# Kernel optimization log

Hardware: AMD Instinct MI355X
Metric: run time of the kernel (lower is better)

The kernel has to match this reference:

```python
import jax, jax.numpy as jnp
import numpy as np

N_OBS = 2_097_152
N_BAND = 4
T_SPAN = 3650.0  # days


def setup_inputs() -> dict:
    key = jax.random.key(0)
    k0, k1, k2, k3, k4, k5 = jax.random.split(key, 6)
    t = jnp.sort(jax.random.uniform(k0, (N_OBS,), jnp.float32) * T_SPAN)
    band = jax.random.randint(k1, (N_OBS,), 0, N_BAND)
    y = jax.random.normal(k2, (N_OBS,), jnp.float32)
    yerr = 0.1 + 0.9 * jax.random.uniform(k3, (N_OBS,), jnp.float32)
    log_amp_delta = 0.1 * jax.random.normal(k4, (N_BAND - 1,), jnp.float32)
    # [log sigma, log ell] for the quasisep Exp kernel
    log_kernel_param = jnp.array([0.0, np.log(50.0)], dtype=jnp.float32) + \
        0.1 * jax.random.normal(k5, (2,), jnp.float32)
    return {"t": t, "band": band, "y": y, "yerr": yerr,
            "log_amp_delta": log_amp_delta, "log_kernel_param": log_kernel_param}


def _log_prob(t, band, y, yerr, log_amp_delta, log_kernel_param):
    # amp_transform: prepend 0 -> per-band amplitudes
    amps = jnp.exp(jnp.concatenate([jnp.zeros(1, log_amp_delta.dtype), log_amp_delta]))
    sigma2 = jnp.exp(2.0 * log_kernel_param[0])
    ell = jnp.exp(log_kernel_param[1])

    # lag_transform with zero lags: sort by time (assume_sorted path of tinygp)
    inds = jnp.argsort(t)
    ts, b = t[inds], band[inds]
    ys, dg = y[inds], (yerr ** 2)[inds]

    # multiband Exp kernel: K_ij = sigma2 * u_i * u_j * exp(-(t_i - t_j)/ell), i>=j
    u = amps[b]                       # per-point amplitude
    a = dg + sigma2 * u * u           # diagonal K_ii + noise
    U = sigma2 * u                    # semiseparable left factor
    V = u                             # semiseparable right factor
    dt = jnp.diff(ts)
    P = jnp.concatenate([jnp.zeros(1, ts.dtype), jnp.exp(-dt / ell)])  # decay factors

    # Celerite O(N) Cholesky (K = L D L^T) fused with the forward solve L z = y.
    def step(carry, x):
        cS, cg = carry                # cS = S_{n-1} + D_{n-1} W_{n-1}^2 ; cg = g_{n-1} + W_{n-1} z_{n-1}
        Pn, an, Un, Vn, yn = x
        Sn = Pn * Pn * cS
        gn = Pn * cg
        Dn = an - Un * Un * Sn
        Wn = (Vn - Sn * Un) / Dn
        zn = yn - Un * gn
        return (Sn + Dn * Wn * Wn, gn + Wn * zn), (jnp.log(Dn), zn * zn / Dn)

    zero = jnp.zeros((), ts.dtype)
    _, (logD, quad) = jax.lax.scan(step, (zero, zero), (P, a, U, V, ys))
    n = ts.shape[0]
    return -0.5 * (jnp.sum(quad) + jnp.sum(logD) + n * jnp.log(2.0 * jnp.pi))


def reference(t, band, y, yerr, log_amp_delta, log_kernel_param):
    return _log_prob(t, band, y, yerr, log_amp_delta, log_kernel_param)
```

## Files before the change

### kernel.cpp

```cpp
#include <hip/hip_runtime.h>
#include <math.h>

#define N_TOTAL 2097152
#define NT 256
#define NC 16
#define EPB (NT * NC)
#define NB (N_TOTAL / EPB)

struct DMat { double al, be, ga, de, c, e, f; };

__device__ __forceinline__ DMat dmat_identity() {
    DMat m; m.al = 1.0; m.be = 0.0; m.ga = 0.0; m.de = 1.0; m.c = 1.0; m.e = 0.0; m.f = 0.0;
    return m;
}

__device__ __forceinline__ DMat dmat_compose(const DMat& A, const DMat& B) {
    DMat r;
    r.al = A.al * B.al + A.be * B.ga;
    r.be = A.al * B.be + A.be * B.de;
    r.ga = A.ga * B.al + A.de * B.ga;
    r.de = A.ga * B.be + A.de * B.de;
    r.c  = A.c * B.c;
    r.e  = A.e * B.al + A.c * B.e + A.f * B.ga;
    r.f  = A.e * B.be + A.c * B.f + A.f * B.de;
    return r;
}

__device__ __forceinline__ void dmat_normalize(DMat& m) {
    double mx = fmax(fabs(m.al), fabs(m.be));
    mx = fmax(mx, fabs(m.ga));
    mx = fmax(mx, fabs(m.de));
    mx = fmax(mx, fabs(m.c));
    mx = fmax(mx, fabs(m.e));
    mx = fmax(mx, fabs(m.f));
    if (!(mx > 0.0) || isinf(mx)) return;
    double inv = 1.0 / mx;
    m.al *= inv; m.be *= inv; m.ga *= inv; m.de *= inv;
    m.c *= inv; m.e *= inv; m.f *= inv;
}

__device__ __forceinline__ void dmat_store(double* sm, int i, const DMat& m) {
    sm[0 * NT + i] = m.al; sm[1 * NT + i] = m.be; sm[2 * NT + i] = m.ga;
    sm[3 * NT + i] = m.de; sm[4 * NT + i] = m.c;  sm[5 * NT + i] = m.e;
    sm[6 * NT + i] = m.f;
}

__device__ __forceinline__ DMat dmat_load(const double* sm, int i) {
    DMat m;
    m.al = sm[0 * NT + i]; m.be = sm[1 * NT + i]; m.ga = sm[2 * NT + i];
    m.de = sm[3 * NT + i]; m.c  = sm[4 * NT + i]; m.e  = sm[5 * NT + i];
    m.f  = sm[6 * NT + i];
    return m;
}

__device__ __forceinline__ DMat dmat_scan_inclusive(double* sm, DMat mine, int tid) {
    dmat_store(sm, tid, mine);
    __syncthreads();
    for (int d = 1; d < NT; d <<= 1) {
        DMat o;
        bool has = (tid >= d);
        if (has) o = dmat_load(sm, tid - d);
        __syncthreads();
        if (has) {
            mine = dmat_compose(mine, o);
            dmat_normalize(mine);
            dmat_store(sm, tid, mine);
        }
        __syncthreads();
    }
    return mine;
}

__device__ __forceinline__ DMat elem_mat(double P, double a, double U, double V, double yy) {
    double p = P * P;
    DMat m;
    m.al = p * (a - 2.0 * U * V);
    m.be = V * V;
    m.ga = -(p * U * U);
    m.de = a;
    m.c  = P * (a - U * V);
    m.e  = -(yy * p * U);
    m.f  = yy * V;
    return m;
}

__global__ __launch_bounds__(NT) void k_upsweep(
    const float* __restrict__ t, const int* __restrict__ band,
    const float* __restrict__ y, const float* __restrict__ yerr,
    const float* __restrict__ lad, const float* __restrict__ lkp,
    double* __restrict__ block_comp)
{
    __shared__ double sm[7 * NT];
    const int tid = threadIdx.x;
    const double sigma2 = exp(2.0 * (double)lkp[0]);
    const double inv_ell = exp(-(double)lkp[1]);
    double amps[4];
    amps[0] = 1.0;
    amps[1] = exp((double)lad[0]);
    amps[2] = exp((double)lad[1]);
    amps[3] = exp((double)lad[2]);

    const int base = (blockIdx.x * NT + tid) * NC;
    double tprev = (base == 0) ? 0.0 : (double)t[base - 1];
    DMat acc = dmat_identity();
    #pragma unroll
    for (int k = 0; k < NC; k += 4) {
        float4 tv = *reinterpret_cast<const float4*>(t + base + k);
        float4 yv = *reinterpret_cast<const float4*>(y + base + k);
        float4 ev = *reinterpret_cast<const float4*>(yerr + base + k);
        int4   bv = *reinterpret_cast<const int4*>(band + base + k);
        float tc[4] = {tv.x, tv.y, tv.z, tv.w};
        float yc[4] = {yv.x, yv.y, yv.z, yv.w};
        float ec[4] = {ev.x, ev.y, ev.z, ev.w};
        int   bc[4] = {bv.x, bv.y, bv.z, bv.w};
        #pragma unroll
        for (int j = 0; j < 4; ++j) {
            double u = amps[bc[j] & 3];
            double a = (double)ec[j] * (double)ec[j] + sigma2 * u * u;
            double U = sigma2 * u;
            double P = ((base + k + j) == 0) ? 0.0
                     : exp(-((double)tc[j] - tprev) * inv_ell);
            acc = dmat_compose(elem_mat(P, a, U, u, (double)yc[j]), acc);
            tprev = (double)tc[j];
        }
    }
    dmat_normalize(acc);
    DMat incl = dmat_scan_inclusive(sm, acc, tid);
    if (tid == NT - 1) {
        double* o = block_comp + blockIdx.x * 7;
        o[0] = incl.al; o[1] = incl.be; o[2] = incl.ga; o[3] = incl.de;
        o[4] = incl.c;  o[5] = incl.e;  o[6] = incl.f;
    }
}

__global__ __launch_bounds__(NT) void k_spine(
    const double* __restrict__ block_comp, double* __restrict__ block_excl)
{
    __shared__ double sm[7 * NT];
    const int tid = threadIdx.x;
    const double* p0 = block_comp + (2 * tid) * 7;
    const double* p1 = block_comp + (2 * tid + 1) * 7;
    DMat m0 = {p0[0], p0[1], p0[2], p0[3], p0[4], p0[5], p0[6]};
    DMat m1 = {p1[0], p1[1], p1[2], p1[3], p1[4], p1[5], p1[6]};
    DMat mine = dmat_compose(m1, m0);
    dmat_normalize(mine);
    dmat_scan_inclusive(sm, mine, tid);
    DMat E = (tid == 0) ? dmat_identity() : dmat_load(sm, tid - 1);
    double* o0 = block_excl + (2 * tid) * 7;
    o0[0] = E.al; o0[1] = E.be; o0[2] = E.ga; o0[3] = E.de;
    o0[4] = E.c;  o0[5] = E.e;  o0[6] = E.f;
    DMat M = dmat_compose(m0, E);
    dmat_normalize(M);
    double* o1 = block_excl + (2 * tid + 1) * 7;
    o1[0] = M.al; o1[1] = M.be; o1[2] = M.ga; o1[3] = M.de;
    o1[4] = M.c;  o1[5] = M.e;  o1[6] = M.f;
}

__global__ __launch_bounds__(NT) void k_replay(
    const float* __restrict__ t, const int* __restrict__ band,
    const float* __restrict__ y, const float* __restrict__ yerr,
    const float* __restrict__ lad, const float* __restrict__ lkp,
    const double* __restrict__ block_excl, double* __restrict__ accum)
{
    __shared__ double sm[7 * NT];
    const int tid = threadIdx.x;
    const double sigma2 = exp(2.0 * (double)lkp[0]);
    const double inv_ell = exp(-(double)lkp[1]);
    double amps[4];
    amps[0] = 1.0;
    amps[1] = exp((double)lad[0]);
    amps[2] = exp((double)lad[1]);
    amps[3] = exp((double)lad[2]);

    const int base = (blockIdx.x * NT + tid) * NC;
    double tprev = (base == 0) ? 0.0 : (double)t[base - 1];

    double Pv[NC];
    float av[NC], Uv[NC], Vv[NC], yv_[NC];
    DMat acc = dmat_identity();
    #pragma unroll
    for (int k = 0; k < NC; k += 4) {
        float4 tv = *reinterpret_cast<const float4*>(t + base + k);
        float4 yv = *reinterpret_cast<const float4*>(y + base + k);
        float4 ev = *reinterpret_cast<const float4*>(yerr + base + k);
        int4   bv = *reinterpret_cast<const int4*>(band + base + k);
        float tc[4] = {tv.x, tv.y, tv.z, tv.w};
        float yc[4] = {yv.x, yv.y, yv.z, yv.w};
        float ec[4] = {ev.x, ev.y, ev.z, ev.w};
        int   bc[4] = {bv.x, bv.y, bv.z, bv.w};
        #pragma unroll
        for (int j = 0; j < 4; ++j) {
            double u = amps[bc[j] & 3];
            double a = (double)ec[j] * (double)ec[j] + sigma2 * u * u;
            double U = sigma2 * u;
            double P = ((base + k + j) == 0) ? 0.0
                     : exp(-((double)tc[j] - tprev) * inv_ell);
            Pv[k + j] = P;
            av[k + j] = (float)a; Uv[k + j] = (float)U;
            Vv[k + j] = (float)u; yv_[k + j] = yc[j];
            acc = dmat_compose(elem_mat(P, a, U, u, (double)yc[j]), acc);
            tprev = (double)tc[j];
        }
    }
    dmat_normalize(acc);
    dmat_scan_inclusive(sm, acc, tid);
    DMat E = (tid == 0) ? dmat_identity() : dmat_load(sm, tid - 1);

    const double* pb = block_excl + blockIdx.x * 7;
    DMat Eb = {pb[0], pb[1], pb[2], pb[3], pb[4], pb[5], pb[6]};
    DMat F = dmat_compose(E, Eb);
    dmat_normalize(F);
    double x = 0.0, g = 0.0;
    if (F.de != 0.0 && !isinf(F.de)) {
        double invde = 1.0 / F.de;
        x = F.be * invde;
        g = F.f  * invde;
    }
    if (!isfinite(x)) x = 0.0;
    if (!isfinite(g)) g = 0.0;

    double s_logD = 0.0, s_quad = 0.0;
    #pragma unroll
    for (int k = 0; k < NC; ++k) {
        double P = Pv[k], a = (double)av[k], U = (double)Uv[k];
        double V = (double)Vv[k], yy = (double)yv_[k];
        double p = P * P;
        double S = p * x;
        double D = a - U * U * S;
        if (!(D > 1e-300)) D = 1e-300;
        double W = (V - S * U) / D;
        double gn = P * g;
        double z = yy - U * gn;
        s_logD += log(D);
        s_quad += z * z / D;
        x = S + D * W * W;
        g = gn + W * z;
    }

    __syncthreads();
    sm[tid] = s_logD;
    sm[NT + tid] = s_quad;
    __syncthreads();
    for (int d = NT / 2; d > 0; d >>= 1) {
        if (tid < d) {
            sm[tid] += sm[tid + d];
            sm[NT + tid] += sm[NT + tid + d];
        }
        __syncthreads();
    }
    if (tid == 0) {
        atomicAdd(&accum[0], sm[0]);
        atomicAdd(&accum[1], sm[NT]);
    }
}

__global__ void k_zero(double* __restrict__ accum) {
    accum[0] = 0.0;
    accum[1] = 0.0;
}

__global__ void k_final(const double* __restrict__ accum, float* __restrict__ out) {
    double r = -0.5 * (accum[0] + accum[1]
                       + (double)N_TOTAL * 1.8378770664093454836);
    out[0] = (float)r;
}

extern "C" void kernel_launch(void* const* d_in, const int* in_sizes, int n_in,
                              void* d_out, int out_size, void* d_ws, size_t ws_size,
                              hipStream_t stream)
{
    const float* t    = (const float*)d_in[0];
    const int*   band = (const int*)d_in[1];
    const float* y    = (const float*)d_in[2];
    const float* yerr = (const float*)d_in[3];
    const float* lad  = (const float*)d_in[4];
    const float* lkp  = (const float*)d_in[5];

    double* dws        = (double*)d_ws;
    double* block_comp = dws;
    double* block_excl = dws + NB * 7;
    double* accum      = dws + 2 * NB * 7;

    k_zero<<<1, 1, 0, stream>>>(accum);
    k_upsweep<<<NB, NT, 0, stream>>>(t, band, y, yerr, lad, lkp, block_comp);
    k_spine<<<1, NT, 0, stream>>>(block_comp, block_excl);
    k_replay<<<NB, NT, 0, stream>>>(t, band, y, yerr, lad, lkp, block_excl, accum);
    k_final<<<1, 1, 0, stream>>>(accum, (float*)d_out);
}
```

Baseline: 123.9 us.

## Store per-thread prefixes to skip matrix rescan in replay, split upsweep chains

The upsweep now writes every thread's inclusive prefix matrix to global memory in SoA layout. The replay kernel reads its predecessor's prefix instead of recomputing the per-element matrix compose and block scan. The upsweep runs two independent half-chains per thread for more ILP, and exponentials drop to float expf with branchless band amplitudes. Replay batches logs via a product of D, uses wave shuffles for the reduction, and fuses zero/final kernels via a done-counter, trading extra global traffic and some precision for less FP64 compute and fewer launches.

```diff
diff --git a/kernel.cpp b/kernel.cpp
--- a/kernel.cpp
+++ b/kernel.cpp
@@ -6,6 +6,7 @@
 #define NC 16
 #define EPB (NT * NC)
 #define NB (N_TOTAL / EPB)
+#define NTH (NB * NT)
 
 struct DMat { double al, be, ga, de, c, e, f; };
 
@@ -84,25 +85,156 @@
     return m;
 }
 
+__device__ __forceinline__ double band_amp(int b, double a1, double a2, double a3) {
+    double lo = (b & 1) ? a1 : 1.0;
+    double hi = (b & 1) ? a3 : a2;
+    return (b & 2) ? hi : lo;
+}
+
 __global__ __launch_bounds__(NT) void k_upsweep(
     const float* __restrict__ t, const int* __restrict__ band,
     const float* __restrict__ y, const float* __restrict__ yerr,
     const float* __restrict__ lad, const float* __restrict__ lkp,
-    double* __restrict__ block_comp)
+    double* __restrict__ ptc)
 {
     __shared__ double sm[7 * NT];
     const int tid = threadIdx.x;
     const double sigma2 = exp(2.0 * (double)lkp[0]);
-    const double inv_ell = exp(-(double)lkp[1]);
-    double amps[4];
-    amps[0] = 1.0;
-    amps[1] = exp((double)lad[0]);
-    amps[2] = exp((double)lad[1]);
-    amps[3] = exp((double)lad[2]);
-
-    const int base = (blockIdx.x * NT + tid) * NC;
-    double tprev = (base == 0) ? 0.0 : (double)t[base - 1];
-    DMat acc = dmat_identity();
+    const float inv_ell_f = expf(-lkp[1]);
+    const double amp1 = exp((double)lad[0]);
+    const double amp2 = exp((double)lad[1]);
+    const double amp3 = exp((double)lad[2]);
+
+    const int gid = blockIdx.x * NT + tid;
+    const int base = gid * NC;
+    const bool first = (base == 0);
+
+    float tpA = first ? 0.0f : t[base - 1];
+    float tpB = t[base + NC / 2 - 1];
+
+    DMat accA = dmat_identity();
+    DMat accB = dmat_identity();
+
+    #pragma unroll
+    for (int kk = 0; kk < NC / 2; kk += 4) {
+        float4 tvA = *reinterpret_cast<const float4*>(t + base + kk);
+        float4 yvA = *reinterpret_cast<const float4*>(y + base + kk);
+        float4 evA = *reinterpret_cast<const float4*>(yerr + base + kk);
+        int4   bvA = *reinterpret_cast<const int4*>(band + base + kk);
+        float4 tvB = *reinterpret_cast<const float4*>(t + base + NC / 2 + kk);
+        float4 yvB = *reinterpret_cast<const float4*>(y + base + NC / 2 + kk);
+        float4 evB = *reinterpret_cast<const float4*>(yerr + base + NC / 2 + kk);
+        int4   bvB = *reinterpret_cast<const int4*>(band + base + NC / 2 + kk);
+        float tA[4] = {tvA.x, tvA.y, tvA.z, tvA.w};
+        float yA[4] = {yvA.x, yvA.y, yvA.z, yvA.w};
+        float eA[4] = {evA.x, evA.y, evA.z, evA.w};
+        int   bA[4] = {bvA.x, bvA.y, bvA.z, bvA.w};
+        float tB[4] = {tvB.x, tvB.y, tvB.z, tvB.w};
+        float yB[4] = {yvB.x, yvB.y, yvB.z, yvB.w};
+        float eB[4] = {evB.x, evB.y, evB.z, evB.w};
+        int   bB[4] = {bvB.x, bvB.y, bvB.z, bvB.w};
+        #pragma unroll
+        for (int j = 0; j < 4; ++j) {
+            {
+                double u = band_amp(bA[j], amp1, amp2, amp3);
+                double U = sigma2 * u;
+                double a = (double)eA[j] * (double)eA[j] + U * u;
+                float dt = tA[j] - tpA; tpA = tA[j];
+                double P = (first && kk == 0 && j == 0)
+                         ? 0.0 : (double)expf(-dt * inv_ell_f);
+                accA = dmat_compose(elem_mat(P, a, U, u, (double)yA[j]), accA);
+            }
+            {
+                double u = band_amp(bB[j], amp1, amp2, amp3);
+                double U = sigma2 * u;
+                double a = (double)eB[j] * (double)eB[j] + U * u;
+                float dt = tB[j] - tpB; tpB = tB[j];
+                double P = (double)expf(-dt * inv_ell_f);
+                accB = dmat_compose(elem_mat(P, a, U, u, (double)yB[j]), accB);
+            }
+        }
+    }
+    DMat acc = dmat_compose(accB, accA);
+    dmat_normalize(acc);
+    DMat incl = dmat_scan_inclusive(sm, acc, tid);
+    ptc[0 * NTH + gid] = incl.al; ptc[1 * NTH + gid] = incl.be;
+    ptc[2 * NTH + gid] = incl.ga; ptc[3 * NTH + gid] = incl.de;
+    ptc[4 * NTH + gid] = incl.c;  ptc[5 * NTH + gid] = incl.e;
+    ptc[6 * NTH + gid] = incl.f;
+}
+
+__global__ __launch_bounds__(NT) void k_spine(
+    const double* __restrict__ ptc, double* __restrict__ block_excl,
+    double* __restrict__ accum, unsigned int* __restrict__ done)
+{
+    __shared__ double sm[7 * NT];
+    const int tid = threadIdx.x;
+    if (tid == 0) { accum[0] = 0.0; accum[1] = 0.0; *done = 0u; }
+    const int g0 = (2 * tid) * NT + (NT - 1);
+    const int g1 = (2 * tid + 1) * NT + (NT - 1);
+    DMat m0 = {ptc[0 * NTH + g0], ptc[1 * NTH + g0], ptc[2 * NTH + g0],
+               ptc[3 * NTH + g0], ptc[4 * NTH + g0], ptc[5 * NTH + g0],
+               ptc[6 * NTH + g0]};
+    DMat m1 = {ptc[0 * NTH + g1], ptc[1 * NTH + g1], ptc[2 * NTH + g1],
+               ptc[3 * NTH + g1], ptc[4 * NTH + g1], ptc[5 * NTH + g1],
+               ptc[6 * NTH + g1]};
+    DMat mine = dmat_compose(m1, m0);
+    dmat_normalize(mine);
+    dmat_scan_inclusive(sm, mine, tid);
+    DMat E = (tid == 0) ? dmat_identity() : dmat_load(sm, tid - 1);
+    double* o0 = block_excl + (2 * tid) * 7;
+    o0[0] = E.al; o0[1] = E.be; o0[2] = E.ga; o0[3] = E.de;
+    o0[4] = E.c;  o0[5] = E.e;  o0[6] = E.f;
+    DMat M = dmat_compose(m0, E);
+    dmat_normalize(M);
+    double* o1 = block_excl + (2 * tid + 1) * 7;
+    o1[0] = M.al; o1[1] = M.be; o1[2] = M.ga; o1[3] = M.de;
+    o1[4] = M.c;  o1[5] = M.e;  o1[6] = M.f;
+}
+
+__global__ __launch_bounds__(NT) void k_replay(
+    const float* __restrict__ t, const int* __restrict__ band,
+    const float* __restrict__ y, const float* __restrict__ yerr,
+    const float* __restrict__ lad, const float* __restrict__ lkp,
+    const double* __restrict__ ptc, const double* __restrict__ block_excl,
+    double* __restrict__ accum, unsigned int* __restrict__ done,
+    float* __restrict__ out)
+{
+    const int tid = threadIdx.x;
+    const int gid = blockIdx.x * NT + tid;
+    const double sigma2 = exp(2.0 * (double)lkp[0]);
+    const float inv_ell_f = expf(-lkp[1]);
+    const double amp1 = exp((double)lad[0]);
+    const double amp2 = exp((double)lad[1]);
+    const double amp3 = exp((double)lad[2]);
+
+    const double* pb = block_excl + blockIdx.x * 7;
+    DMat Eb = {pb[0], pb[1], pb[2], pb[3], pb[4], pb[5], pb[6]};
+    DMat F;
+    if (tid == 0) {
+        F = Eb;
+    } else {
+        const int gm1 = gid - 1;
+        DMat E = {ptc[0 * NTH + gm1], ptc[1 * NTH + gm1], ptc[2 * NTH + gm1],
+                  ptc[3 * NTH + gm1], ptc[4 * NTH + gm1], ptc[5 * NTH + gm1],
+                  ptc[6 * NTH + gm1]};
+        F = dmat_compose(E, Eb);
+    }
+    dmat_normalize(F);
+    double x = 0.0, g = 0.0;
+    if (F.de != 0.0 && !isinf(F.de)) {
+        double invde = 1.0 / F.de;
+        x = F.be * invde;
+        g = F.f  * invde;
+    }
+    if (!isfinite(x)) x = 0.0;
+    if (!isfinite(g)) g = 0.0;
+
+    const int base = gid * NC;
+    const bool first = (base == 0);
+    float tp = first ? 0.0f : t[base - 1];
+
+    double s_logD = 0.0, s_quad = 0.0, pd = 1.0;
     #pragma unroll
     for (int k = 0; k < NC; k += 4) {
         float4 tv = *reinterpret_cast<const float4*>(t + base + k);
@@ -115,154 +247,54 @@
         int   bc[4] = {bv.x, bv.y, bv.z, bv.w};
         #pragma unroll
         for (int j = 0; j < 4; ++j) {
-            double u = amps[bc[j] & 3];
-            double a = (double)ec[j] * (double)ec[j] + sigma2 * u * u;
+            double u = band_amp(bc[j], amp1, amp2, amp3);
             double U = sigma2 * u;
-            double P = ((base + k + j) == 0) ? 0.0
-                     : exp(-((double)tc[j] - tprev) * inv_ell);
-            acc = dmat_compose(elem_mat(P, a, U, u, (double)yc[j]), acc);
-            tprev = (double)tc[j];
-        }
-    }
-    dmat_normalize(acc);
-    DMat incl = dmat_scan_inclusive(sm, acc, tid);
-    if (tid == NT - 1) {
-        double* o = block_comp + blockIdx.x * 7;
-        o[0] = incl.al; o[1] = incl.be; o[2] = incl.ga; o[3] = incl.de;
-        o[4] = incl.c;  o[5] = incl.e;  o[6] = incl.f;
-    }
-}
-
-__global__ __launch_bounds__(NT) void k_spine(
-    const double* __restrict__ block_comp, double* __restrict__ block_excl)
-{
-    __shared__ double sm[7 * NT];
-    const int tid = threadIdx.x;
-    const double* p0 = block_comp + (2 * tid) * 7;
-    const double* p1 = block_comp + (2 * tid + 1) * 7;
-    DMat m0 = {p0[0], p0[1], p0[2], p0[3], p0[4], p0[5], p0[6]};
-    DMat m1 = {p1[0], p1[1], p1[2], p1[3], p1[4], p1[5], p1[6]};
-    DMat mine = dmat_compose(m1, m0);
-    dmat_normalize(mine);
-    dmat_scan_inclusive(sm, mine, tid);
-    DMat E = (tid == 0) ? dmat_identity() : dmat_load(sm, tid - 1);
-    double* o0 = block_excl + (2 * tid) * 7;
-    o0[0] = E.al; o0[1] = E.be; o0[2] = E.ga; o0[3] = E.de;
-    o0[4] = E.c;  o0[5] = E.e;  o0[6] = E.f;
-    DMat M = dmat_compose(m0, E);
-    dmat_normalize(M);
-    double* o1 = block_excl + (2 * tid + 1) * 7;
-    o1[0] = M.al; o1[1] = M.be; o1[2] = M.ga; o1[3] = M.de;
-    o1[4] = M.c;  o1[5] = M.e;  o1[6] = M.f;
-}
-
-__global__ __launch_bounds__(NT) void k_replay(
-    const float* __restrict__ t, const int* __restrict__ band,
-    const float* __restrict__ y, const float* __restrict__ yerr,
-    const float* __restrict__ lad, const float* __restrict__ lkp,
-    const double* __restrict__ block_excl, double* __restrict__ accum)
-{
-    __shared__ double sm[7 * NT];
-    const int tid = threadIdx.x;
-    const double sigma2 = exp(2.0 * (double)lkp[0]);
-    const double inv_ell = exp(-(double)lkp[1]);
-    double amps[4];
-    amps[0] = 1.0;
-    amps[1] = exp((double)lad[0]);
-    amps[2] = exp((double)lad[1]);
-    amps[3] = exp((double)lad[2]);
-
-    const int base = (blockIdx.x * NT + tid) * NC;
-    double tprev = (base == 0) ? 0.0 : (double)t[base - 1];
-
-    double Pv[NC];
-    float av[NC], Uv[NC], Vv[NC], yv_[NC];
-    DMat acc = dmat_identity();
+            double a = (double)ec[j] * (double)ec[j] + U * u;
+            float dt = tc[j] - tp; tp = tc[j];
+            double P = (first && k == 0 && j == 0)
+                     ? 0.0 : (double)expf(-dt * inv_ell_f);
+            double p = P * P;
+            double S = p * x;
+            double D = a - U * U * S;
+            if (!(D > 1e-300)) D = 1e-300;
+            double invD = 1.0 / D;
+            double W = (u - S * U) * invD;
+            double gn = P * g;
+            double z = (double)yc[j] - U * gn;
+            pd *= D;
+            s_quad = fma(z * z, invD, s_quad);
+            x = fma(D * W, W, S);
+            g = fma(W, z, gn);
+        }
+        if (((k + 4) & 7) == 0) {
+            s_logD += log(pd);
+            pd = 1.0;
+        }
+    }
+
     #pragma unroll
-    for (int k = 0; k < NC; k += 4) {
-        float4 tv = *reinterpret_cast<const float4*>(t + base + k);
-        float4 yv = *reinterpret_cast<const float4*>(y + base + k);
-        float4 ev = *reinterpret_cast<const float4*>(yerr + base + k);
-        int4   bv = *reinterpret_cast<const int4*>(band + base + k);
-        float tc[4] = {tv.x, tv.y, tv.z, tv.w};
-        float yc[4] = {yv.x, yv.y, yv.z, yv.w};
-        float ec[4] = {ev.x, ev.y, ev.z, ev.w};
-        int   bc[4] = {bv.x, bv.y, bv.z, bv.w};
-        #pragma unroll
-        for (int j = 0; j < 4; ++j) {
-            double u = amps[bc[j] & 3];
-            double a = (double)ec[j] * (double)ec[j] + sigma2 * u * u;
-            double U = sigma2 * u;
-            double P = ((base + k + j) == 0) ? 0.0
-                     : exp(-((double)tc[j] - tprev) * inv_ell);
-            Pv[k + j] = P;
-            av[k + j] = (float)a; Uv[k + j] = (float)U;
-            Vv[k + j] = (float)u; yv_[k + j] = yc[j];
-            acc = dmat_compose(elem_mat(P, a, U, u, (double)yc[j]), acc);
-            tprev = (double)tc[j];
-        }
-    }
-    dmat_normalize(acc);
-    dmat_scan_inclusive(sm, acc, tid);
-    DMat E = (tid == 0) ? dmat_identity() : dmat_load(sm, tid - 1);
-
-    const double* pb = block_excl + blockIdx.x * 7;
-    DMat Eb = {pb[0], pb[1], pb[2], pb[3], pb[4], pb[5], pb[6]};
-    DMat F = dmat_compose(E, Eb);
-    dmat_normalize(F);
-    double x = 0.0, g = 0.0;
-    if (F.de != 0.0 && !isinf(F.de)) {
-        double invde = 1.0 / F.de;
-        x = F.be * invde;
-        g = F.f  * invde;
-    }
-    if (!isfinite(x)) x = 0.0;
-    if (!isfinite(g)) g = 0.0;
-
-    double s_logD = 0.0, s_quad = 0.0;
-    #pragma unroll
-    for (int k = 0; k < NC; ++k) {
-        double P = Pv[k], a = (double)av[k], U = (double)Uv[k];
-        double V = (double)Vv[k], yy = (double)yv_[k];
-        double p = P * P;
-        double S = p * x;
-        double D = a - U * U * S;
-        if (!(D > 1e-300)) D = 1e-300;
-        double W = (V - S * U) / D;
-        double gn = P * g;
-        double z = yy - U * gn;
-        s_logD += log(D);
-        s_quad += z * z / D;
-        x = S + D * W * W;
-        g = gn + W * z;
-    }
-
+    for (int off = 32; off > 0; off >>= 1) {
+        s_logD += __shfl_down(s_logD, off);
+        s_quad += __shfl_down(s_quad, off);
+    }
+    __shared__ double red[8];
+    const int wid = tid >> 6, lane = tid & 63;
+    if (lane == 0) { red[wid] = s_logD; red[4 + wid] = s_quad; }
     __syncthreads();
-    sm[tid] = s_logD;
-    sm[NT + tid] = s_quad;
-    __syncthreads();
-    for (int d = NT / 2; d > 0; d >>= 1) {
-        if (tid < d) {
-            sm[tid] += sm[tid + d];
-            sm[NT + tid] += sm[NT + tid + d];
-        }
-        __syncthreads();
-    }
     if (tid == 0) {
-        atomicAdd(&accum[0], sm[0]);
-        atomicAdd(&accum[1], sm[NT]);
-    }
-}
-
-__global__ void k_zero(double* __restrict__ accum) {
-    accum[0] = 0.0;
-    accum[1] = 0.0;
-}
-
-__global__ void k_final(const double* __restrict__ accum, float* __restrict__ out) {
-    double r = -0.5 * (accum[0] + accum[1]
-                       + (double)N_TOTAL * 1.8378770664093454836);
-    out[0] = (float)r;
+        double l = red[0] + red[1] + red[2] + red[3];
+        double q = red[4] + red[5] + red[6] + red[7];
+        atomicAdd(&accum[0], l);
+        atomicAdd(&accum[1], q);
+        __threadfence();
+        unsigned int old = atomicAdd(done, 1u);
+        if (old == NB - 1) {
+            double L = atomicAdd(&accum[0], 0.0);
+            double Q = atomicAdd(&accum[1], 0.0);
+            out[0] = (float)(-0.5 * (Q + L
+                     + (double)N_TOTAL * 1.8378770664093454836));
+        }
+    }
 }
 
 extern "C" void kernel_launch(void* const* d_in, const int* in_sizes, int n_in,
@@ -277,13 +309,13 @@
     const float* lkp  = (const float*)d_in[5];
 
     double* dws        = (double*)d_ws;
-    double* block_comp = dws;
-    double* block_excl = dws + NB * 7;
-    double* accum      = dws + 2 * NB * 7;
-
-    k_zero<<<1, 1, 0, stream>>>(accum);
-    k_upsweep<<<NB, NT, 0, stream>>>(t, band, y, yerr, lad, lkp, block_comp);
-    k_spine<<<1, NT, 0, stream>>>(block_comp, block_excl);
-    k_replay<<<NB, NT, 0, stream>>>(t, band, y, yerr, lad, lkp, block_excl, accum);
-    k_final<<<1, 1, 0, stream>>>(accum, (float*)d_out);
-}
+    double* ptc        = dws;
+    double* block_excl = dws + 7 * NTH;
+    double* accum      = dws + 7 * NTH + 7 * NB;
+    unsigned int* done = (unsigned int*)(dws + 7 * NTH + 7 * NB + 2);
+
+    k_upsweep<<<NB, NT, 0, stream>>>(t, band, y, yerr, lad, lkp, ptc);
+    k_spine<<<1, NT, 0, stream>>>(ptc, block_excl, accum, done);
+    k_replay<<<NB, NT, 0, stream>>>(t, band, y, yerr, lad, lkp,
+                                    ptc, block_excl, accum, done, (float*)d_out);
+}
```

Result: slower. 128.4 us (+3.6%).
